# Kernel tuning notes

Measured on AMD Instinct MI355X. Metric: run time of the kernel, lower is better.

## Reference

```python
import jax, jax.numpy as jnp
import numpy as np

N_EMBD = 1024
N_HEAD = 16
BLOCK_SIZE = 2048
NEG_INF = -1e10


def _rope_cache(head_dim, max_positions):
    # theta_i = 10000^{-2i/dim}, freqs[t, i] = t * theta_i
    theta = 1.0 / (10000.0 ** (jnp.arange(0, head_dim, 2, dtype=jnp.float32) / head_dim))
    freqs = jnp.arange(max_positions, dtype=jnp.float32)[:, None] * theta[None, :]
    return jnp.cos(freqs), jnp.sin(freqs)  # each (max_positions, head_dim//2)


def _apply_rope(x, cos, sin):
    # x: (B, nh, T, hs) interpreted as interleaved complex pairs
    B, nh, T, hs = x.shape
    xr = x.reshape(B, nh, T, hs // 2, 2)
    x0, x1 = xr[..., 0], xr[..., 1]
    c = cos[:T][None, None, :, :]
    s = sin[:T][None, None, :, :]
    o0 = x0 * c - x1 * s
    o1 = x0 * s + x1 * c
    return jnp.stack([o0, o1], axis=-1).reshape(B, nh, T, hs)


def setup_inputs() -> dict:
    key = jax.random.key(0)
    ks = jax.random.split(key, 9)
    B, T, C = 2, 2048, N_EMBD
    sc = 1.0 / np.sqrt(C)
    return {
        "x": jax.random.normal(ks[0], (B, T, C), jnp.float32),
        "Wq": jax.random.normal(ks[1], (C, C), jnp.float32) * sc,
        "bq": jax.random.normal(ks[2], (C,), jnp.float32) * 0.02,
        "Wk": jax.random.normal(ks[3], (C, C), jnp.float32) * sc,
        "bk": jax.random.normal(ks[4], (C,), jnp.float32) * 0.02,
        "Wv": jax.random.normal(ks[5], (C, C), jnp.float32) * sc,
        "bv": jax.random.normal(ks[6], (C,), jnp.float32) * 0.02,
        "Wp": jax.random.normal(ks[7], (C, C), jnp.float32) * sc,
        "bp": jax.random.normal(ks[8], (C,), jnp.float32) * 0.02,
    }


def reference(x, Wq, bq, Wk, bk, Wv, bv, Wp, bp):
    B, T, C = x.shape
    nh, hs = N_HEAD, C // N_HEAD

    def heads(W, b):
        return (x @ W.T + b).reshape(B, T, nh, hs).transpose(0, 2, 1, 3)

    q = heads(Wq, bq)
    k = heads(Wk, bk)
    v = heads(Wv, bv)

    cos, sin = _rope_cache(hs, BLOCK_SIZE)
    q = _apply_rope(q, cos, sin)
    k = _apply_rope(k, cos, sin)

    att = jnp.einsum("bhqd,bhkd->bhqk", q, k) * (1.0 / np.sqrt(hs))
    causal = jnp.tril(jnp.ones((T, T), dtype=bool))
    att = jnp.where(causal[None, None], att, NEG_INF)
    att = jax.nn.softmax(att, axis=-1)
    y = jnp.einsum("bhqk,bhkd->bhqd", att, v)
    y = y.transpose(0, 2, 1, 3).reshape(B, T, C)
    return y @ Wp.T + bp
```

## Files before the change

kernel.cpp:

```cpp
#include <hip/hip_runtime.h>

typedef __bf16 bf16;
typedef short  s16;
typedef s16   s16x8 __attribute__((ext_vector_type(8)));
typedef bf16  bf16x4 __attribute__((ext_vector_type(4)));
typedef float f32x4 __attribute__((ext_vector_type(4)));

#define B_SZ 2
#define T_SEQ 2048
#define C_DIM 1024
#define NH 16
#define HS 64
#define M_TOT (B_SZ * T_SEQ)

#define NEG_BIG (-30000.0f)
#define LOG2_10000 13.287712379549449f
#define Q_PRESCALE 0.18033688011112042f


__device__ __forceinline__ float san(float x) {
    unsigned u = __float_as_uint(x);
    return ((u & 0x7F800000u) == 0x7F800000u) ? 0.f : x;
}

__device__ __forceinline__ void load16_lds(const bf16* g, void* lds_base) {
    __builtin_amdgcn_global_load_lds(
        (const __attribute__((address_space(1))) void*)g,
        (__attribute__((address_space(3))) void*)lds_base, 16, 0, 0);
}

#define CVT_GRID 8448

__global__ __launch_bounds__(256) void cvt_bf16_kernel(
    const float* __restrict__ x,  const float* __restrict__ wq,
    const float* __restrict__ wk, const float* __restrict__ wv,
    const float* __restrict__ wp,
    bf16* __restrict__ xb, bf16* __restrict__ wqb, bf16* __restrict__ wkb,
    bf16* __restrict__ wvb, bf16* __restrict__ wpb,
    float* __restrict__ cs, float* __restrict__ sn)
{
    const int b = blockIdx.x;
    if (b >= 8192) {
        const int idx = (b - 8192) * 256 + threadIdx.x;
        const int t = idx >> 5, i = idx & 31;
        const float theta = __builtin_exp2f(-(float)(2 * i) * (LOG2_10000 / 64.f));
        const float a = (float)t * theta;
        cs[idx] = san(cosf(a));
        sn[idx] = san(sinf(a));
        return;
    }
    int z, base;
    if (b < 4096) { z = 0; base = b; }
    else          { z = 1 + ((b - 4096) >> 10); base = (b - 4096) & 1023; }

    const float* src = (z == 0) ? x : (z == 1) ? wq : (z == 2) ? wk : (z == 3) ? wv : wp;
    bf16* dst = (z == 0) ? xb : (z == 1) ? wqb : (z == 2) ? wkb : (z == 3) ? wvb : wpb;

    const int i = (base * 256 + threadIdx.x) * 4;
    const float4 v = *(const float4*)(src + i);
    bf16x4 o;
    o[0] = (bf16)v.x; o[1] = (bf16)v.y; o[2] = (bf16)v.z; o[3] = (bf16)v.w;
    *(bf16x4*)(dst + i) = o;
}

#define STAGE3(bufi, kk)                                                       \
    load16_lds(gA0 + (kk), (char*)(sA + (bufi) * 2048) + w * 1024);            \
    load16_lds(gB0 + (kk), (char*)(sB + (bufi) * 4096) + w * 1024);            \
    load16_lds(gB1 + (kk), (char*)(sB + (bufi) * 4096) + 4096 + w * 1024);

#define K_STEP3(bufi)                                                          \
    {                                                                          \
        const bf16* pA = sA + (bufi) * 2048;                                   \
        const bf16* pB = sB + (bufi) * 4096;                                   \
        s16x8 af[2], bfr[4];                                                   \
        _Pragma("unroll")                                                      \
        for (int mt = 0; mt < 2; mt++)                                         \
            af[mt] = *(const s16x8*)(pA + (wm * 32 + mt * 16 + r) * 32 + qs * 8); \
        _Pragma("unroll")                                                      \
        for (int nt = 0; nt < 4; nt++)                                         \
            bfr[nt] = *(const s16x8*)(pB + (wn * 64 + nt * 16 + r) * 32 + qs * 8); \
        _Pragma("unroll")                                                      \
        for (int mt = 0; mt < 2; mt++)                                         \
            _Pragma("unroll")                                                  \
            for (int nt = 0; nt < 4; nt++)                                     \
                acc[mt][nt] = __builtin_amdgcn_mfma_f32_16x16x32_bf16(         \
                    af[mt], bfr[nt], acc[mt][nt], 0, 0, 0);                    \
    }

#define GEMM_CORE(Xp, Wp_)                                                     \
    const int t = threadIdx.x;                                                 \
    const int w = t >> 6;                                                      \
    const int lane = t & 63;                                                   \
    const int qd = lane >> 4;                                                  \
    const int r  = lane & 15;                                                  \
    const int qs = qd ^ ((r >> 1) & 3);                                        \
    const int wm = w & 1, wn = w >> 1;                                         \
    const int srow = t >> 2;                                                   \
    const int scol = ((t & 3) ^ ((t >> 3) & 3)) * 8;                           \
    const bf16* gA0 = (Xp) + (size_t)(m0 + srow) * C_DIM + scol;               \
    const bf16* gB0 = (Wp_) + (size_t)(n0 + srow) * C_DIM + scol;              \
    const bf16* gB1 = (Wp_) + (size_t)(n0 + 64 + srow) * C_DIM + scol;         \
    f32x4 acc[2][4] = {};                                                      \
    STAGE3(0, 0)                                                               \
    STAGE3(1, 32)                                                              \
    _Pragma("unroll")                                                          \
    for (int kt_ = 0; kt_ < 32; kt_++) {                                       \
        __builtin_amdgcn_sched_barrier(0);                                     \
        if (kt_ < 30) asm volatile("s_waitcnt vmcnt(3) lgkmcnt(0)" ::: "memory"); \
        else          asm volatile("s_waitcnt vmcnt(0) lgkmcnt(0)" ::: "memory"); \
        __builtin_amdgcn_sched_barrier(0);                                     \
        __builtin_amdgcn_s_barrier();                                          \
        __builtin_amdgcn_sched_barrier(0);                                     \
        if (kt_ + 2 < 32) { STAGE3((kt_ + 2) % 3, (kt_ + 2) * 32) }            \
        K_STEP3(kt_ % 3)                                                       \
    }

__global__ __launch_bounds__(256) void qkv_gemm(
    const bf16* __restrict__ X,
    const bf16* __restrict__ Wq, const float* __restrict__ bq,
    const bf16* __restrict__ Wk, const float* __restrict__ bk,
    const bf16* __restrict__ Wv, const float* __restrict__ bv,
    const float* __restrict__ cs_tab, const float* __restrict__ sn_tab,
    bf16* __restrict__ q_ws, bf16* __restrict__ k_ws, bf16* __restrict__ vt_ws)
{
    __shared__ __attribute__((aligned(16))) bf16 sA[3 * 64 * 32];
    __shared__ __attribute__((aligned(16))) bf16 sB[3 * 128 * 32];

    const int mode = blockIdx.z;
    const bf16*  Wm   = (mode == 0) ? Wq : (mode == 1) ? Wk : Wv;
    const float* bias = (mode == 0) ? bq : (mode == 1) ? bk : bv;
    const int m0 = blockIdx.x * 64;
    const int n0 = blockIdx.y * 128;

    GEMM_CORE(X, Wm)

    if (mode == 2) {
        #pragma unroll
        for (int mt = 0; mt < 2; mt++) {
            const int mrow0 = m0 + wm * 32 + mt * 16 + qd * 4;
            const int bb = mrow0 >> 11;
            const int t0 = mrow0 & 2047;
            #pragma unroll
            for (int nt = 0; nt < 4; nt++) {
                const int col = n0 + wn * 64 + nt * 16 + r;
                const int h = col >> 6, d = col & 63;
                const float bv_ = bias[col];
                bf16x4 pk;
                #pragma unroll
                for (int reg = 0; reg < 4; reg++)
                    pk[reg] = (bf16)san(acc[mt][nt][reg] + bv_);
                *(bf16x4*)(vt_ws + ((size_t)(bb * NH + h) * HS + d) * T_SEQ + t0) = pk;
            }
        }
    } else {
        bf16* out = (mode == 0) ? q_ws : k_ws;
        const float post = (mode == 0) ? Q_PRESCALE : 1.0f;
        #pragma unroll
        for (int mt = 0; mt < 2; mt++) {
            const int mrow0 = m0 + wm * 32 + mt * 16 + qd * 4;
            const int bb = mrow0 >> 11;
            const int t0 = mrow0 & 2047;
            #pragma unroll
            for (int nt = 0; nt < 4; nt++) {
                const int col = n0 + wn * 64 + nt * 16 + r;
                const int h = col >> 6, d = col & 63;
                const int pi = d >> 1;
                const float bv_ = bias[col];
                #pragma unroll
                for (int reg = 0; reg < 4; reg++) {
                    const int tt = t0 + reg;
                    float v = san(acc[mt][nt][reg] + bv_);
                    float partner = __shfl_xor(v, 1);
                    float c = cs_tab[tt * 32 + pi];
                    float s = sn_tab[tt * 32 + pi];
                    float rot = (d & 1) ? (v * c + partner * s)
                                        : (v * c - partner * s);
                    out[((size_t)(bb * NH + h) * T_SEQ + tt) * HS + d] =
                        (bf16)san(rot * post);
                }
            }
        }
    }
}

__global__ __launch_bounds__(256) void proj_gemm(
    const bf16* __restrict__ Y, const bf16* __restrict__ Wp,
    const float* __restrict__ bp, float* __restrict__ out)
{
    __shared__ __attribute__((aligned(16))) bf16 sA[3 * 64 * 32];
    __shared__ __attribute__((aligned(16))) bf16 sB[3 * 128 * 32];

    const int m0 = blockIdx.x * 64;
    const int n0 = blockIdx.y * 128;

    GEMM_CORE(Y, Wp)

    #pragma unroll
    for (int mt = 0; mt < 2; mt++) {
        const int mrow0 = m0 + wm * 32 + mt * 16 + qd * 4;
        #pragma unroll
        for (int nt = 0; nt < 4; nt++) {
            const int col = n0 + wn * 64 + nt * 16 + r;
            const float bv_ = bp[col];
            #pragma unroll
            for (int reg = 0; reg < 4; reg++)
                out[(size_t)(mrow0 + reg) * C_DIM + col] = san(acc[mt][nt][reg] + bv_);
        }
    }
}

__global__ __launch_bounds__(256) void attn_kernel(
    const bf16* __restrict__ q_ws, const bf16* __restrict__ k_ws,
    const bf16* __restrict__ vt_ws, bf16* __restrict__ y_ws)
{
    __shared__ __attribute__((aligned(16))) bf16 sK[2][2][64][32];
    __shared__ __attribute__((aligned(16))) bf16 sV[2][2][64][32];
    __shared__ __attribute__((aligned(16))) bf16 sP[4][16][72];

    const int id = (int)(blockIdx.x + gridDim.x * blockIdx.y);
    const int bh = (id & 7) + 8 * (id >> 7);
    const int bx = (id >> 3) & 15;

    const int w    = threadIdx.x >> 6;
    const int lane = threadIdx.x & 63;
    const int qd = lane >> 4;
    const int r  = lane & 15;
    const int qs = qd ^ ((r >> 1) & 3);

    const bf16* Qb = q_ws + (size_t)bh * T_SEQ * HS;
    const bf16* Kb = k_ws + (size_t)bh * T_SEQ * HS;
    const bf16* Vb = vt_ws + (size_t)bh * HS * T_SEQ;

    const int srow = lane >> 2;
    const int scol = ((lane & 3) ^ ((lane >> 3) & 3)) * 8;
    const bf16* Kb_w = Kb + (size_t)(w * 16 + srow) * HS + scol;
    const bf16* Vb_w = Vb + (size_t)(w * 16 + srow) * T_SEQ + scol;

    bf16 (*pw)[72] = sP[w];
    const int bb = bh >> 4, h = bh & 15;

    #pragma unroll 1
    for (int phase = 0; phase < 2; phase++) {
        const int qt = phase ? bx : (T_SEQ / 64 - 1 - bx);
        const int q0 = qt * 64 + w * 16;

        s16x8 aq0 = *(const s16x8*)(Qb + (size_t)(q0 + r) * HS + qd * 8);
        s16x8 aq1 = *(const s16x8*)(Qb + (size_t)(q0 + r) * HS + 32 + qd * 8);

        f32x4 o[4] = {};
        float l_lane = 0.f;

        __syncthreads();
        load16_lds(Kb_w,      &sK[0][0][w * 16][0]);
        load16_lds(Kb_w + 32, &sK[0][1][w * 16][0]);
        load16_lds(Vb_w,      &sV[0][0][w * 16][0]);
        load16_lds(Vb_w + 32, &sV[0][1][w * 16][0]);

        for (int kt = 0; kt <= qt; kt++) {
            const int cur = kt & 1;
            __syncthreads();

            if (kt < qt) {
                const bf16* kp = Kb_w + (size_t)(kt + 1) * 64 * HS;
                const bf16* vp = Vb_w + (kt + 1) * 64;
                load16_lds(kp,      &sK[cur ^ 1][0][w * 16][0]);
                load16_lds(kp + 32, &sK[cur ^ 1][1][w * 16][0]);
                load16_lds(vp,      &sV[cur ^ 1][0][w * 16][0]);
                load16_lds(vp + 32, &sV[cur ^ 1][1][w * 16][0]);
            }

            f32x4 s[4];
            #pragma unroll
            for (int c = 0; c < 4; c++) {
                s16x8 k0 = *(const s16x8*)&sK[cur][0][c * 16 + r][qs * 8];
                s16x8 k1 = *(const s16x8*)&sK[cur][1][c * 16 + r][qs * 8];
                f32x4 z = {};
                z = __builtin_amdgcn_mfma_f32_16x16x32_bf16(k0, aq0, z, 0, 0, 0);
                z = __builtin_amdgcn_mfma_f32_16x16x32_bf16(k1, aq1, z, 0, 0, 0);
                s[c] = z;
            }

            if (kt == qt) {
                const int qg = q0 + r;
                #pragma unroll
                for (int c = 0; c < 4; c++)
                    #pragma unroll
                    for (int reg = 0; reg < 4; reg++) {
                        const int kg = kt * 64 + c * 16 + qd * 4 + reg;
                        s[c][reg] = (kg <= qg) ? s[c][reg] : NEG_BIG;
                    }
            }

            #pragma unroll
            for (int c = 0; c < 4; c++) {
                bf16x4 pk;
                #pragma unroll
                for (int reg = 0; reg < 4; reg++) {
                    float p = __builtin_exp2f(s[c][reg]);
                    l_lane += p;
                    pk[reg] = (bf16)p;
                }
                *(bf16x4*)&pw[r][c * 16 + qd * 4] = pk;
            }

            s16x8 ap0 = *(const s16x8*)&pw[r][qd * 8];
            s16x8 ap1 = *(const s16x8*)&pw[r][32 + qd * 8];
            #pragma unroll
            for (int nt = 0; nt < 4; nt++) {
                s16x8 av0 = *(const s16x8*)&sV[cur][0][nt * 16 + r][qs * 8];
                s16x8 av1 = *(const s16x8*)&sV[cur][1][nt * 16 + r][qs * 8];
                o[nt] = __builtin_amdgcn_mfma_f32_16x16x32_bf16(av0, ap0, o[nt], 0, 0, 0);
                o[nt] = __builtin_amdgcn_mfma_f32_16x16x32_bf16(av1, ap1, o[nt], 0, 0, 0);
            }
        }

        float l = l_lane;
        l += __shfl_xor(l, 16);
        l += __shfl_xor(l, 32);
        const float inv = 1.f / fmaxf(l, 1e-20f);

        const int q = q0 + r;
        bf16* dst = y_ws + ((size_t)(bb * T_SEQ + q) * NH + h) * HS;
        #pragma unroll
        for (int nt = 0; nt < 4; nt++) {
            bf16x4 pk;
            #pragma unroll
            for (int reg = 0; reg < 4; reg++)
                pk[reg] = (bf16)san(o[nt][reg] * inv);
            *(bf16x4*)(dst + nt * 16 + qd * 4) = pk;
        }
    }
}

extern "C" void kernel_launch(void* const* d_in, const int* in_sizes, int n_in,
                              void* d_out, int out_size, void* d_ws, size_t ws_size,
                              hipStream_t stream)
{
    const size_t MB = 1024 * 1024;
    const size_t NEED = 40 * MB + 2 * 65536 * sizeof(float);
    if (ws_size < NEED || n_in < 9) return;

    const float* x  = (const float*)d_in[0];
    const float* Wq = (const float*)d_in[1];
    const float* bq = (const float*)d_in[2];
    const float* Wk = (const float*)d_in[3];
    const float* bk = (const float*)d_in[4];
    const float* Wv = (const float*)d_in[5];
    const float* bv = (const float*)d_in[6];
    const float* Wp = (const float*)d_in[7];
    const float* bp = (const float*)d_in[8];
    float* out = (float*)d_out;

    char* ws = (char*)d_ws;
    bf16*  q_ws   = (bf16*)(ws + 0 * MB);
    bf16*  k_ws   = (bf16*)(ws + 8 * MB);
    bf16*  vt_ws  = (bf16*)(ws + 16 * MB);
    bf16*  x_b    = (bf16*)(ws + 24 * MB);
    bf16*  y_ws   = (bf16*)(ws + 24 * MB);
    bf16*  Wq_b   = (bf16*)(ws + 32 * MB);
    bf16*  Wk_b   = (bf16*)(ws + 34 * MB);
    bf16*  Wv_b   = (bf16*)(ws + 36 * MB);
    bf16*  Wp_b   = (bf16*)(ws + 38 * MB);
    float* cs_tab = (float*)(ws + 40 * MB);
    float* sn_tab = cs_tab + 65536;

    cvt_bf16_kernel<<<dim3(CVT_GRID), 256, 0, stream>>>(
        x, Wq, Wk, Wv, Wp, x_b, Wq_b, Wk_b, Wv_b, Wp_b, cs_tab, sn_tab);
    qkv_gemm<<<dim3(M_TOT / 64, C_DIM / 128, 3), 256, 0, stream>>>(
        x_b, Wq_b, bq, Wk_b, bk, Wv_b, bv, cs_tab, sn_tab, q_ws, k_ws, vt_ws);
    attn_kernel<<<dim3(T_SEQ / 128, B_SZ * NH), 256, 0, stream>>>(
        q_ws, k_ws, vt_ws, y_ws);
    proj_gemm<<<dim3(M_TOT / 64, C_DIM / 128), 256, 0, stream>>>(
        y_ws, Wp_b, bp, out);
}
```

Before: 200.4 us.

## Use 256x256 tiles with 512 threads in fused QKV GEMM

New measurement: 188.8 us. -5.8%, faster.

```diff
diff --git a/kernel.cpp b/kernel.cpp
--- a/kernel.cpp
+++ b/kernel.cpp
@@ -61,6 +61,121 @@
     bf16x4 o;
     o[0] = (bf16)v.x; o[1] = (bf16)v.y; o[2] = (bf16)v.z; o[3] = (bf16)v.w;
     *(bf16x4*)(dst + i) = o;
+}
+
+#define QSTAGE(bufi, kk)                                                       \
+    load16_lds(gA + (kk),               (char*)(sA[bufi]) + w * 1024);         \
+    load16_lds(gA + 128 * C_DIM + (kk), (char*)(sA[bufi]) + 8192 + w * 1024);  \
+    load16_lds(gB + (kk),               (char*)(sB[bufi]) + w * 1024);         \
+    load16_lds(gB + 128 * C_DIM + (kk), (char*)(sB[bufi]) + 8192 + w * 1024);
+
+__global__ __launch_bounds__(512, 2) void qkv_gemm(
+    const bf16* __restrict__ X, const bf16* __restrict__ W_all,
+    const float* __restrict__ bq, const float* __restrict__ bk,
+    const float* __restrict__ bv,
+    const float* __restrict__ cs_tab, const float* __restrict__ sn_tab,
+    bf16* __restrict__ q_ws, bf16* __restrict__ k_ws, bf16* __restrict__ vt_ws)
+{
+    __shared__ __attribute__((aligned(16))) bf16 sA[3][256 * 32];
+    __shared__ __attribute__((aligned(16))) bf16 sB[3][256 * 32];
+
+    const int m0 = blockIdx.x * 256;
+    const int n0 = blockIdx.y * 256;
+    const int mode = blockIdx.y >> 2;
+
+    const int t = threadIdx.x;
+    const int w = t >> 6;
+    const int lane = t & 63;
+    const int qd = lane >> 4;
+    const int r  = lane & 15;
+    const int qs = qd ^ ((r >> 1) & 3);
+    const int wm = w >> 2, wn = w & 3;
+    const int srow = t >> 2;
+    const int scol = ((t & 3) ^ ((t >> 3) & 3)) * 8;
+    const bf16* gA = X + (size_t)(m0 + srow) * C_DIM + scol;
+    const bf16* gB = W_all + (size_t)(n0 + srow) * C_DIM + scol;
+
+    f32x4 acc[8][4] = {};
+
+    QSTAGE(0, 0)
+    QSTAGE(1, 32)
+    #pragma unroll
+    for (int kt_ = 0; kt_ < 32; kt_++) {
+        __builtin_amdgcn_sched_barrier(0);
+        if (kt_ < 30) asm volatile("s_waitcnt vmcnt(4) lgkmcnt(0)" ::: "memory");
+        else          asm volatile("s_waitcnt vmcnt(0) lgkmcnt(0)" ::: "memory");
+        __builtin_amdgcn_sched_barrier(0);
+        __builtin_amdgcn_s_barrier();
+        __builtin_amdgcn_sched_barrier(0);
+        if (kt_ + 2 < 32) { QSTAGE((kt_ + 2) % 3, (kt_ + 2) * 32) }
+        {
+            const bf16* pA = sA[kt_ % 3];
+            const bf16* pB = sB[kt_ % 3];
+            s16x8 af[8], bfr[4];
+            #pragma unroll
+            for (int mt = 0; mt < 8; mt++)
+                af[mt] = *(const s16x8*)(pA + (wm * 128 + mt * 16 + r) * 32 + qs * 8);
+            #pragma unroll
+            for (int nt = 0; nt < 4; nt++)
+                bfr[nt] = *(const s16x8*)(pB + (wn * 64 + nt * 16 + r) * 32 + qs * 8);
+            #pragma unroll
+            for (int mt = 0; mt < 8; mt++)
+                #pragma unroll
+                for (int nt = 0; nt < 4; nt++)
+                    acc[mt][nt] = __builtin_amdgcn_mfma_f32_16x16x32_bf16(
+                        af[mt], bfr[nt], acc[mt][nt], 0, 0, 0);
+        }
+    }
+
+    const float* bias = (mode == 0) ? bq : (mode == 1) ? bk : bv;
+
+    if (mode == 2) {
+        #pragma unroll
+        for (int mt = 0; mt < 8; mt++) {
+            const int mrow0 = m0 + wm * 128 + mt * 16 + qd * 4;
+            const int bb = mrow0 >> 11;
+            const int t0 = mrow0 & 2047;
+            #pragma unroll
+            for (int nt = 0; nt < 4; nt++) {
+                const int cm = (n0 & 1023) + wn * 64 + nt * 16 + r;
+                const int h = cm >> 6, d = cm & 63;
+                const float bv_ = bias[cm];
+                bf16x4 pk;
+                #pragma unroll
+                for (int reg = 0; reg < 4; reg++)
+                    pk[reg] = (bf16)san(acc[mt][nt][reg] + bv_);
+                *(bf16x4*)(vt_ws + ((size_t)(bb * NH + h) * HS + d) * T_SEQ + t0) = pk;
+            }
+        }
+    } else {
+        bf16* out = (mode == 0) ? q_ws : k_ws;
+        const float post = (mode == 0) ? Q_PRESCALE : 1.0f;
+        #pragma unroll
+        for (int mt = 0; mt < 8; mt++) {
+            const int mrow0 = m0 + wm * 128 + mt * 16 + qd * 4;
+            const int bb = mrow0 >> 11;
+            const int t0 = mrow0 & 2047;
+            #pragma unroll
+            for (int nt = 0; nt < 4; nt++) {
+                const int cm = (n0 & 1023) + wn * 64 + nt * 16 + r;
+                const int h = cm >> 6, d = cm & 63;
+                const int pi = d >> 1;
+                const float bv_ = bias[cm];
+                #pragma unroll
+                for (int reg = 0; reg < 4; reg++) {
+                    const int tt = t0 + reg;
+                    float v = san(acc[mt][nt][reg] + bv_);
+                    float partner = __shfl_xor(v, 1);
+                    float c = cs_tab[tt * 32 + pi];
+                    float s = sn_tab[tt * 32 + pi];
+                    float rot = (d & 1) ? (v * c + partner * s)
+                                        : (v * c - partner * s);
+                    out[((size_t)(bb * NH + h) * T_SEQ + tt) * HS + d] =
+                        (bf16)san(rot * post);
+                }
+            }
+        }
+    }
 }
 
 #define STAGE3(bufi, kk)                                                       \
@@ -115,74 +230,6 @@
         K_STEP3(kt_ % 3)                                                       \
     }
 
-__global__ __launch_bounds__(256) void qkv_gemm(
-    const bf16* __restrict__ X,
-    const bf16* __restrict__ Wq, const float* __restrict__ bq,
-    const bf16* __restrict__ Wk, const float* __restrict__ bk,
-    const bf16* __restrict__ Wv, const float* __restrict__ bv,
-    const float* __restrict__ cs_tab, const float* __restrict__ sn_tab,
-    bf16* __restrict__ q_ws, bf16* __restrict__ k_ws, bf16* __restrict__ vt_ws)
-{
-    __shared__ __attribute__((aligned(16))) bf16 sA[3 * 64 * 32];
-    __shared__ __attribute__((aligned(16))) bf16 sB[3 * 128 * 32];
-
-    const int mode = blockIdx.z;
-    const bf16*  Wm   = (mode == 0) ? Wq : (mode == 1) ? Wk : Wv;
-    const float* bias = (mode == 0) ? bq : (mode == 1) ? bk : bv;
-    const int m0 = blockIdx.x * 64;
-    const int n0 = blockIdx.y * 128;
-
-    GEMM_CORE(X, Wm)
-
-    if (mode == 2) {
-        #pragma unroll
-        for (int mt = 0; mt < 2; mt++) {
-            const int mrow0 = m0 + wm * 32 + mt * 16 + qd * 4;
-            const int bb = mrow0 >> 11;
-            const int t0 = mrow0 & 2047;
-            #pragma unroll
-            for (int nt = 0; nt < 4; nt++) {
-                const int col = n0 + wn * 64 + nt * 16 + r;
-                const int h = col >> 6, d = col & 63;
-                const float bv_ = bias[col];
-                bf16x4 pk;
-                #pragma unroll
-                for (int reg = 0; reg < 4; reg++)
-                    pk[reg] = (bf16)san(acc[mt][nt][reg] + bv_);
-                *(bf16x4*)(vt_ws + ((size_t)(bb * NH + h) * HS + d) * T_SEQ + t0) = pk;
-            }
-        }
-    } else {
-        bf16* out = (mode == 0) ? q_ws : k_ws;
-        const float post = (mode == 0) ? Q_PRESCALE : 1.0f;
-        #pragma unroll
-        for (int mt = 0; mt < 2; mt++) {
-            const int mrow0 = m0 + wm * 32 + mt * 16 + qd * 4;
-            const int bb = mrow0 >> 11;
-            const int t0 = mrow0 & 2047;
-            #pragma unroll
-            for (int nt = 0; nt < 4; nt++) {
-                const int col = n0 + wn * 64 + nt * 16 + r;
-                const int h = col >> 6, d = col & 63;
-                const int pi = d >> 1;
-                const float bv_ = bias[col];
-                #pragma unroll
-                for (int reg = 0; reg < 4; reg++) {
-                    const int tt = t0 + reg;
-                    float v = san(acc[mt][nt][reg] + bv_);
-                    float partner = __shfl_xor(v, 1);
-                    float c = cs_tab[tt * 32 + pi];
-                    float s = sn_tab[tt * 32 + pi];
-                    float rot = (d & 1) ? (v * c + partner * s)
-                                        : (v * c - partner * s);
-                    out[((size_t)(bb * NH + h) * T_SEQ + tt) * HS + d] =
-                        (bf16)san(rot * post);
-                }
-            }
-        }
-    }
-}
-
 __global__ __launch_bounds__(256) void proj_gemm(
     const bf16* __restrict__ Y, const bf16* __restrict__ Wp,
     const float* __restrict__ bp, float* __restrict__ out)
@@ -363,11 +410,12 @@
     bf16*  Wp_b   = (bf16*)(ws + 38 * MB);
     float* cs_tab = (float*)(ws + 40 * MB);
     float* sn_tab = cs_tab + 65536;
+    const bf16* W_all = Wq_b;
 
     cvt_bf16_kernel<<<dim3(CVT_GRID), 256, 0, stream>>>(
         x, Wq, Wk, Wv, Wp, x_b, Wq_b, Wk_b, Wv_b, Wp_b, cs_tab, sn_tab);
-    qkv_gemm<<<dim3(M_TOT / 64, C_DIM / 128, 3), 256, 0, stream>>>(
-        x_b, Wq_b, bq, Wk_b, bk, Wv_b, bv, cs_tab, sn_tab, q_ws, k_ws, vt_ws);
+    qkv_gemm<<<dim3(M_TOT / 256, 3 * C_DIM / 256), 512, 0, stream>>>(
+        x_b, W_all, bq, bk, bv, cs_tab, sn_tab, q_ws, k_ws, vt_ws);
     attn_kernel<<<dim3(T_SEQ / 128, B_SZ * NH), 256, 0, stream>>>(
         q_ws, k_ws, vt_ws, y_ws);
     proj_gemm<<<dim3(M_TOT / 64, C_DIM / 128), 256, 0, stream>>>(
```
